# Kernel tuning notes

Measured on AMD Instinct MI355X. Metric: run time of the kernel, lower is better.

The kernel has to match this reference:

```python
import jax, jax.numpy as jnp
import numpy as np

D_MODEL = 1024
N_HEADS = 16
D_K = D_MODEL // N_HEADS

def setup_inputs() -> dict:
    key = jax.random.key(0)
    ks = jax.random.split(key, 9)
    s = 1.0 / np.sqrt(D_MODEL)
    inp = {"x": jax.random.normal(ks[0], (2, 2048, D_MODEL), dtype=jnp.float32)}
    for i, name in enumerate(["q", "k", "v", "o"]):
        inp[f"W{name}"] = jax.random.uniform(ks[1 + i], (D_MODEL, D_MODEL), dtype=jnp.float32, minval=-s, maxval=s)
        inp[f"b{name}"] = jax.random.uniform(ks[5 + i], (D_MODEL,), dtype=jnp.float32, minval=-s, maxval=s)
    return inp

def _split_heads(t):
    B, S, _ = t.shape
    return t.reshape(B, S, N_HEADS, D_K).transpose(0, 2, 1, 3)  # [B,H,S,d_k]

def reference(x, Wq, bq, Wk, bk, Wv, bv, Wo, bo):
    # QKV projections (torch Linear: x @ W.T + b)
    q = _split_heads(x @ Wq.T + bq)
    k = _split_heads(x @ Wk.T + bk)
    v = _split_heads(x @ Wv.T + bv)
    scores = jnp.einsum('bhqd,bhkd->bhqk', q, k) / jnp.sqrt(jnp.asarray(D_K, x.dtype))
    probs = jax.nn.softmax(scores, axis=-1)
    attn = jnp.einsum('bhqk,bhkd->bhqd', probs, v)  # [B,H,S,d_k]
    B, H, S, _ = attn.shape
    merged = attn.transpose(0, 2, 1, 3).reshape(B, S, D_MODEL)
    return merged @ Wo.T + bo
```

## Files before the change

kernel.cpp:

```cpp
#include <hip/hip_runtime.h>
#include <hip/hip_bf16.h>
#include <stdint.h>


#define LOG2E 1.4426950408889634f

typedef float f32x4 __attribute__((ext_vector_type(4)));
typedef float f32x16 __attribute__((ext_vector_type(16)));
typedef short bf16x8 __attribute__((ext_vector_type(8)));
typedef short bf16x4 __attribute__((ext_vector_type(4)));
typedef unsigned int u32x2 __attribute__((ext_vector_type(2)));

__device__ __forceinline__ unsigned short f2bf(float f) {
  __hip_bfloat16 h = __float2bfloat16(f);
  return reinterpret_cast<unsigned short&>(h);
}

#define GLDS(g, l) __builtin_amdgcn_global_load_lds(                          \
    (const __attribute__((address_space(1))) void*)(g),                       \
    (__attribute__((address_space(3))) void*)(l), 16, 0, 0)

__global__ __launch_bounds__(256) void k_conv(const float* __restrict__ src,
                                              unsigned short* __restrict__ dst,
                                              int n4, float scale) {
  int i = blockIdx.x * 256 + threadIdx.x;
  const int stride = gridDim.x * 256;
  for (; i < n4; i += stride) {
    float4 v = ((const float4*)src)[i];
    ushort4 o;
    o.x = f2bf(v.x * scale);
    o.y = f2bf(v.y * scale);
    o.z = f2bf(v.z * scale);
    o.w = f2bf(v.w * scale);
    ((ushort4*)dst)[i] = o;
  }
}

__global__ __launch_bounds__(256) void k_convW(const float* __restrict__ wq,
                                               const float* __restrict__ wk,
                                               const float* __restrict__ wv,
                                               const float* __restrict__ wo,
                                               unsigned short* __restrict__ dq,
                                               unsigned short* __restrict__ dk,
                                               unsigned short* __restrict__ dv,
                                               unsigned short* __restrict__ dw) {
  const int m = blockIdx.y;
  const float* src = (m == 0) ? wq : (m == 1) ? wk : (m == 2) ? wv : wo;
  unsigned short* dst = (m == 0) ? dq : (m == 1) ? dk : (m == 2) ? dv : dw;
  const float scale = (m == 0) ? (0.125f * LOG2E) : 1.0f;
  int i = blockIdx.x * 256 + threadIdx.x;
  float4 v = ((const float4*)src)[i];
  ushort4 o;
  o.x = f2bf(v.x * scale);
  o.y = f2bf(v.y * scale);
  o.z = f2bf(v.z * scale);
  o.w = f2bf(v.w * scale);
  ((ushort4*)dst)[i] = o;
}

__global__ __launch_bounds__(256) void k_bias(const float* __restrict__ bq,
                                              const float* __restrict__ bk,
                                              const float* __restrict__ bv,
                                              float* __restrict__ out) {
  int i = blockIdx.x * 256 + threadIdx.x;
  float v;
  if (i < 1024) v = bq[i] * (0.125f * LOG2E);
  else if (i < 2048) v = bk[i - 1024];
  else v = bv[i - 2048];
  out[i] = v;
}

template <int MODE>
__global__ __launch_bounds__(256) void k_gemm(const unsigned short* __restrict__ A,
                                              const unsigned short* __restrict__ B,
                                              const float* __restrict__ bias,
                                              void* __restrict__ outp) {
  __shared__ unsigned short As[128 * 32];
  __shared__ unsigned short Bs[128 * 32];
  const int tid = threadIdx.x;
  const int lane = tid & 63, wid = tid >> 6;
  const int wr = wid >> 1, wc = wid & 1;
  const int r = lane & 15, g = lane >> 4;
  const int bm = blockIdx.x, bn = blockIdx.y;

  const unsigned short* gA = A + (size_t)bm * 128 * 1024;
  const unsigned short* gB = B + (size_t)bn * 128 * 1024;
  const int row0 = tid >> 2, cg = (tid & 3) * 8;

  f32x4 acc[4][4] = {};

  for (int k0 = 0; k0 < 1024; k0 += 32) {
    __syncthreads();
    GLDS(gA + (size_t)row0 * 1024 + k0 + cg,        As + row0 * 32 + cg);
    GLDS(gA + (size_t)(row0 + 64) * 1024 + k0 + cg, As + (row0 + 64) * 32 + cg);
    GLDS(gB + (size_t)row0 * 1024 + k0 + cg,        Bs + row0 * 32 + cg);
    GLDS(gB + (size_t)(row0 + 64) * 1024 + k0 + cg, Bs + (row0 + 64) * 32 + cg);
    __syncthreads();

    bf16x8 af[4], bfr[4];
#pragma unroll
    for (int i = 0; i < 4; i++) {
      af[i]  = *(const bf16x8*)(As + (wr * 64 + i * 16 + r) * 32 + g * 8);
      bfr[i] = *(const bf16x8*)(Bs + (wc * 64 + i * 16 + r) * 32 + g * 8);
    }
#pragma unroll
    for (int i = 0; i < 4; i++)
#pragma unroll
      for (int j = 0; j < 4; j++)
        acc[i][j] = __builtin_amdgcn_mfma_f32_16x16x32_bf16(af[i], bfr[j], acc[i][j], 0, 0, 0);
  }

#pragma unroll
  for (int i = 0; i < 4; i++) {
    const int rowb = bm * 128 + wr * 64 + i * 16 + g * 4;
#pragma unroll
    for (int j = 0; j < 4; j++) {
      const int col = bn * 128 + wc * 64 + j * 16 + r;
      const float bv = bias[col];
#pragma unroll
      for (int t = 0; t < 4; t++) {
        const int row = rowb + t;
        const float val = acc[i][j][t] + bv;
        if (MODE == 0) {
          const int mat = col >> 10, nn = col & 1023;
          const int hh = nn >> 6, dd = nn & 63;
          const int bb = row >> 11, ss = row & 2047;
          size_t idx;
          if (mat == 2)
            idx = (size_t)2 * 4194304 + (size_t)((bb * 16 + hh) * 64 + dd) * 2048 + ss;
          else
            idx = (size_t)mat * 4194304 + (size_t)((bb * 16 + hh) * 2048 + ss) * 64 + dd;
          ((unsigned short*)outp)[idx] = f2bf(val);
        } else {
          ((float*)outp)[(size_t)row * 1024 + col] = val;
        }
      }
    }
  }
}

__global__ __launch_bounds__(256) void k_attn(const unsigned short* __restrict__ Q,
                                              const unsigned short* __restrict__ Km,
                                              const unsigned short* __restrict__ Vt,
                                              unsigned short* __restrict__ merged) {
  __shared__ unsigned short Kb[2][4096];
  __shared__ unsigned short Vb[2][4096];
  const int tid = threadIdx.x;
  const int lane = tid & 63, w = tid >> 6;
  const int l31 = lane & 31, hi = lane >> 5;
  const int bh = blockIdx.y;
  const int b = bh >> 4, h = bh & 15;
  const int q0 = blockIdx.x * 128;

  const unsigned short* Qh  = Q  + (size_t)bh * 131072;
  const unsigned short* Kh  = Km + (size_t)bh * 131072;
  const unsigned short* Vth = Vt + (size_t)bh * 131072;

  const int qrow = q0 + w * 32 + l31;
  bf16x8 bQ[4];
#pragma unroll
  for (int c = 0; c < 4; c++)
    bQ[c] = *(const bf16x8*)(Qh + (size_t)qrow * 64 + c * 16 + hi * 8);

  int ksrc[2], vsrc[2];
#pragma unroll
  for (int op = 0; op < 2; op++) {
    const int ck = op * 256 + tid;
    const int s = ck >> 8, c = (ck >> 6) & 3, l2 = ck & 63;
    ksrc[op] = (s * 32 + (l2 & 31)) * 64 + c * 16 + (l2 >> 5) * 8;
    vsrc[op] = (s * 32 + (l2 & 31)) * 2048 + c * 16 + (l2 >> 5) * 8;
  }
  const int ldst = tid * 8;

  GLDS(Kh + ksrc[0],  &Kb[0][ldst]);
  GLDS(Kh + ksrc[1],  &Kb[0][2048 + ldst]);
  GLDS(Vth + vsrc[0], &Vb[0][ldst]);
  GLDS(Vth + vsrc[1], &Vb[0][2048 + ldst]);
  __syncthreads();

  f32x16 o0 = {0.f,0.f,0.f,0.f,0.f,0.f,0.f,0.f,0.f,0.f,0.f,0.f,0.f,0.f,0.f,0.f};
  f32x16 o1 = o0;
  float lsum = 0.f;

  for (int t = 0; t < 32; ++t) {
    const int cur = t & 1;
    if (t < 31) {
      const size_t kv = (size_t)(t + 1) * 64;
      GLDS(Kh + kv * 64 + ksrc[0],  &Kb[cur ^ 1][ldst]);
      GLDS(Kh + kv * 64 + ksrc[1],  &Kb[cur ^ 1][2048 + ldst]);
      GLDS(Vth + kv + vsrc[0], &Vb[cur ^ 1][ldst]);
      GLDS(Vth + kv + vsrc[1], &Vb[cur ^ 1][2048 + ldst]);
    }

    bf16x8 kf[2][4], vf[2][4];
#pragma unroll
    for (int s = 0; s < 2; s++)
#pragma unroll
      for (int c = 0; c < 4; c++) {
        kf[s][c] = *(const bf16x8*)(&Kb[cur][((s * 4 + c) * 64 + lane) * 8]);
        vf[s][c] = *(const bf16x8*)(&Vb[cur][((s * 4 + c) * 64 + lane) * 8]);
      }

    f32x16 z = {0.f,0.f,0.f,0.f,0.f,0.f,0.f,0.f,0.f,0.f,0.f,0.f,0.f,0.f,0.f,0.f};
    f32x16 St0 = z, St1 = z;
#pragma unroll
    for (int c = 0; c < 4; c++) {
      St0 = __builtin_amdgcn_mfma_f32_32x32x16_bf16(kf[0][c], bQ[c], St0, 0, 0, 0);
      St1 = __builtin_amdgcn_mfma_f32_32x32x16_bf16(kf[1][c], bQ[c], St1, 0, 0, 0);
    }

    float p0[16], p1[16];
    float ps = 0.f;
#pragma unroll
    for (int u = 0; u < 16; u++) {
      p0[u] = __builtin_amdgcn_exp2f(St0[u]);
      p1[u] = __builtin_amdgcn_exp2f(St1[u]);
      ps += p0[u] + p1[u];
    }
    lsum += ps;

#pragma unroll
    for (int c = 0; c < 4; c++) {
      const float* pp = (c < 2) ? p0 : p1;
      const int R = (c & 1) * 8;
      unsigned int a0, a1, b0, b1;
      asm("v_cvt_pk_bf16_f32 %0, %1, %2" : "=v"(a0) : "v"(pp[R + 0]), "v"(pp[R + 1]));
      asm("v_cvt_pk_bf16_f32 %0, %1, %2" : "=v"(a1) : "v"(pp[R + 2]), "v"(pp[R + 3]));
      asm("v_cvt_pk_bf16_f32 %0, %1, %2" : "=v"(b0) : "v"(pp[R + 4]), "v"(pp[R + 5]));
      asm("v_cvt_pk_bf16_f32 %0, %1, %2" : "=v"(b1) : "v"(pp[R + 6]), "v"(pp[R + 7]));
      u32x2 r0 = __builtin_amdgcn_permlane32_swap(a0, b0, false, false);
      u32x2 r1 = __builtin_amdgcn_permlane32_swap(a1, b1, false, false);
      union { unsigned int u[4]; bf16x8 v; } pf;
      pf.u[0] = r0[0]; pf.u[1] = r1[0]; pf.u[2] = r0[1]; pf.u[3] = r1[1];
      o0 = __builtin_amdgcn_mfma_f32_32x32x16_bf16(vf[0][c], pf.v, o0, 0, 0, 0);
      o1 = __builtin_amdgcn_mfma_f32_32x32x16_bf16(vf[1][c], pf.v, o1, 0, 0, 0);
    }

    __syncthreads();
  }

  const float inv = 1.0f / (lsum + __shfl_xor(lsum, 32));
  const size_t base = (size_t)(b * 2048 + qrow) * 1024 + h * 64;
#pragma unroll
  for (int ds = 0; ds < 2; ds++) {
    const f32x16& oo = ds ? o1 : o0;
#pragma unroll
    for (int m = 0; m < 4; m++) {
      bf16x4 ov;
#pragma unroll
      for (int i = 0; i < 4; i++) ov[i] = (short)f2bf(oo[m * 4 + i] * inv);
      *(bf16x4*)(&merged[base + ds * 32 + m * 8 + hi * 4]) = ov;
    }
  }
}

extern "C" void kernel_launch(void* const* d_in, const int* in_sizes, int n_in,
                              void* d_out, int out_size, void* d_ws, size_t ws_size,
                              hipStream_t stream) {
  const float* x  = (const float*)d_in[0];
  const float* Wq = (const float*)d_in[1];
  const float* bq = (const float*)d_in[2];
  const float* Wk = (const float*)d_in[3];
  const float* bk = (const float*)d_in[4];
  const float* Wv = (const float*)d_in[5];
  const float* bv = (const float*)d_in[6];
  const float* Wo = (const float*)d_in[7];
  const float* bo = (const float*)d_in[8];

  if (ws_size < (size_t)50343936) return;

  unsigned short* ws  = (unsigned short*)d_ws;
  unsigned short* xb  = ws;
  unsigned short* Wb  = ws + 4194304;
  unsigned short* Wob = ws + 7340032;
  unsigned short* qkv = ws + 8388608;
  unsigned short* mrg = ws + 20971520;
  float* biasQ = (float*)(ws + 25165824);

  k_conv<<<dim3(2048), dim3(256), 0, stream>>>(x, xb, 1048576, 1.0f);
  k_convW<<<dim3(1024, 4), dim3(256), 0, stream>>>(Wq, Wk, Wv, Wo,
      Wb, Wb + 1048576, Wb + 2097152, Wob);
  k_bias<<<dim3(12), dim3(256), 0, stream>>>(bq, bk, bv, biasQ);

  k_gemm<0><<<dim3(32, 24), dim3(256), 0, stream>>>(xb, Wb, biasQ, (void*)qkv);
  k_attn<<<dim3(16, 32), dim3(256), 0, stream>>>(qkv, qkv + 4194304, qkv + 8388608, mrg);
  k_gemm<1><<<dim3(32, 8), dim3(256), 0, stream>>>(mrg, Wob, bo, d_out);
}
```

Before: 134.0 us.

## Split attention KV range across two warp groups with LDS reduction

The attention kernel now launches 512 threads per block, and two groups of four waves each process half of the key/value sequence for the same 128 query rows. Partial outputs and row sums are combined through a swizzled LDS buffer before normalization and store. The inner loop is also restructured into per-32-key subtiles to cut live registers. This doubles waves per block to hide latency, at the cost of more LDS, an extra reduction phase and block-wide barriers shared by both groups.

```diff
diff --git a/kernel.cpp b/kernel.cpp
--- a/kernel.cpp
+++ b/kernel.cpp
@@ -139,22 +139,23 @@
   }
 }
 
-__global__ __launch_bounds__(256) void k_attn(const unsigned short* __restrict__ Q,
-                                              const unsigned short* __restrict__ Km,
-                                              const unsigned short* __restrict__ Vt,
-                                              unsigned short* __restrict__ merged) {
-  __shared__ unsigned short Kb[2][4096];
-  __shared__ unsigned short Vb[2][4096];
+__global__ __launch_bounds__(512, 4) void k_attn(const unsigned short* __restrict__ Q,
+                                                 const unsigned short* __restrict__ Km,
+                                                 const unsigned short* __restrict__ Vt,
+                                                 unsigned short* __restrict__ merged) {
+  __shared__ unsigned short Kb[2][2][4096];
+  __shared__ unsigned short Vb[2][2][4096];
   const int tid = threadIdx.x;
-  const int lane = tid & 63, w = tid >> 6;
+  const int kg = tid >> 8, gtid = tid & 255;
+  const int lane = tid & 63, w = (tid >> 6) & 3;
   const int l31 = lane & 31, hi = lane >> 5;
   const int bh = blockIdx.y;
   const int b = bh >> 4, h = bh & 15;
   const int q0 = blockIdx.x * 128;
 
   const unsigned short* Qh  = Q  + (size_t)bh * 131072;
-  const unsigned short* Kh  = Km + (size_t)bh * 131072;
-  const unsigned short* Vth = Vt + (size_t)bh * 131072;
+  const unsigned short* KhG = Km + (size_t)bh * 131072 + (size_t)kg * 65536;
+  const unsigned short* VtG = Vt + (size_t)bh * 131072 + 1024 * kg;
 
   const int qrow = q0 + w * 32 + l31;
   bf16x8 bQ[4];
@@ -165,91 +166,132 @@
   int ksrc[2], vsrc[2];
 #pragma unroll
   for (int op = 0; op < 2; op++) {
-    const int ck = op * 256 + tid;
+    const int ck = op * 256 + gtid;
     const int s = ck >> 8, c = (ck >> 6) & 3, l2 = ck & 63;
     ksrc[op] = (s * 32 + (l2 & 31)) * 64 + c * 16 + (l2 >> 5) * 8;
     vsrc[op] = (s * 32 + (l2 & 31)) * 2048 + c * 16 + (l2 >> 5) * 8;
   }
-  const int ldst = tid * 8;
-
-  GLDS(Kh + ksrc[0],  &Kb[0][ldst]);
-  GLDS(Kh + ksrc[1],  &Kb[0][2048 + ldst]);
-  GLDS(Vth + vsrc[0], &Vb[0][ldst]);
-  GLDS(Vth + vsrc[1], &Vb[0][2048 + ldst]);
+  const int ldst = gtid * 8;
+
+  GLDS(KhG + ksrc[0], &Kb[kg][0][ldst]);
+  GLDS(KhG + ksrc[1], &Kb[kg][0][2048 + ldst]);
+  GLDS(VtG + vsrc[0], &Vb[kg][0][ldst]);
+  GLDS(VtG + vsrc[1], &Vb[kg][0][2048 + ldst]);
   __syncthreads();
 
   f32x16 o0 = {0.f,0.f,0.f,0.f,0.f,0.f,0.f,0.f,0.f,0.f,0.f,0.f,0.f,0.f,0.f,0.f};
   f32x16 o1 = o0;
   float lsum = 0.f;
 
-  for (int t = 0; t < 32; ++t) {
+  for (int t = 0; t < 16; ++t) {
     const int cur = t & 1;
-    if (t < 31) {
+    if (t < 15) {
       const size_t kv = (size_t)(t + 1) * 64;
-      GLDS(Kh + kv * 64 + ksrc[0],  &Kb[cur ^ 1][ldst]);
-      GLDS(Kh + kv * 64 + ksrc[1],  &Kb[cur ^ 1][2048 + ldst]);
-      GLDS(Vth + kv + vsrc[0], &Vb[cur ^ 1][ldst]);
-      GLDS(Vth + kv + vsrc[1], &Vb[cur ^ 1][2048 + ldst]);
-    }
-
-    bf16x8 kf[2][4], vf[2][4];
-#pragma unroll
-    for (int s = 0; s < 2; s++)
-#pragma unroll
-      for (int c = 0; c < 4; c++) {
-        kf[s][c] = *(const bf16x8*)(&Kb[cur][((s * 4 + c) * 64 + lane) * 8]);
-        vf[s][c] = *(const bf16x8*)(&Vb[cur][((s * 4 + c) * 64 + lane) * 8]);
+      GLDS(KhG + kv * 64 + ksrc[0], &Kb[kg][cur ^ 1][ldst]);
+      GLDS(KhG + kv * 64 + ksrc[1], &Kb[kg][cur ^ 1][2048 + ldst]);
+      GLDS(VtG + kv + vsrc[0], &Vb[kg][cur ^ 1][ldst]);
+      GLDS(VtG + kv + vsrc[1], &Vb[kg][cur ^ 1][2048 + ldst]);
+    }
+
+    const unsigned short* kb = &Kb[kg][cur][0];
+    const unsigned short* vb = &Vb[kg][cur][0];
+
+#define SUBTILE(SC)                                                            \
+    {                                                                          \
+      bf16x8 kf0 = *(const bf16x8*)(kb + (((SC)*4 + 0) * 64 + lane) * 8);      \
+      bf16x8 kf1 = *(const bf16x8*)(kb + (((SC)*4 + 1) * 64 + lane) * 8);      \
+      bf16x8 kf2 = *(const bf16x8*)(kb + (((SC)*4 + 2) * 64 + lane) * 8);      \
+      bf16x8 kf3 = *(const bf16x8*)(kb + (((SC)*4 + 3) * 64 + lane) * 8);      \
+      f32x16 St = {0.f,0.f,0.f,0.f,0.f,0.f,0.f,0.f,                            \
+                   0.f,0.f,0.f,0.f,0.f,0.f,0.f,0.f};                           \
+      St = __builtin_amdgcn_mfma_f32_32x32x16_bf16(kf0, bQ[0], St, 0, 0, 0);   \
+      St = __builtin_amdgcn_mfma_f32_32x32x16_bf16(kf1, bQ[1], St, 0, 0, 0);   \
+      St = __builtin_amdgcn_mfma_f32_32x32x16_bf16(kf2, bQ[2], St, 0, 0, 0);   \
+      St = __builtin_amdgcn_mfma_f32_32x32x16_bf16(kf3, bQ[3], St, 0, 0, 0);   \
+      float p[16];                                                             \
+      float ps = 0.f;                                                          \
+      _Pragma("unroll")                                                        \
+      for (int u = 0; u < 16; u++) {                                           \
+        p[u] = __builtin_amdgcn_exp2f(St[u]);                                  \
+        ps += p[u];                                                            \
+      }                                                                        \
+      lsum += ps;                                                              \
+      unsigned int a0, a1, b0, b1;                                             \
+      asm("v_cvt_pk_bf16_f32 %0, %1, %2" : "=v"(a0) : "v"(p[0]), "v"(p[1]));   \
+      asm("v_cvt_pk_bf16_f32 %0, %1, %2" : "=v"(a1) : "v"(p[2]), "v"(p[3]));   \
+      asm("v_cvt_pk_bf16_f32 %0, %1, %2" : "=v"(b0) : "v"(p[4]), "v"(p[5]));   \
+      asm("v_cvt_pk_bf16_f32 %0, %1, %2" : "=v"(b1) : "v"(p[6]), "v"(p[7]));   \
+      u32x2 r0 = __builtin_amdgcn_permlane32_swap(a0, b0, false, false);       \
+      u32x2 r1 = __builtin_amdgcn_permlane32_swap(a1, b1, false, false);       \
+      union { unsigned int u[4]; bf16x8 v; } pfE;                              \
+      pfE.u[0] = r0[0]; pfE.u[1] = r1[0]; pfE.u[2] = r0[1]; pfE.u[3] = r1[1];  \
+      asm("v_cvt_pk_bf16_f32 %0, %1, %2" : "=v"(a0) : "v"(p[8]), "v"(p[9]));   \
+      asm("v_cvt_pk_bf16_f32 %0, %1, %2" : "=v"(a1) : "v"(p[10]), "v"(p[11])); \
+      asm("v_cvt_pk_bf16_f32 %0, %1, %2" : "=v"(b0) : "v"(p[12]), "v"(p[13])); \
+      asm("v_cvt_pk_bf16_f32 %0, %1, %2" : "=v"(b1) : "v"(p[14]), "v"(p[15])); \
+      r0 = __builtin_amdgcn_permlane32_swap(a0, b0, false, false);             \
+      r1 = __builtin_amdgcn_permlane32_swap(a1, b1, false, false);             \
+      union { unsigned int u[4]; bf16x8 v; } pfO;                              \
+      pfO.u[0] = r0[0]; pfO.u[1] = r1[0]; pfO.u[2] = r0[1]; pfO.u[3] = r1[1];  \
+      bf16x8 v00 = *(const bf16x8*)(vb + ((0 + 2*(SC)) * 64 + lane) * 8);      \
+      bf16x8 v01 = *(const bf16x8*)(vb + ((1 + 2*(SC)) * 64 + lane) * 8);      \
+      bf16x8 v10 = *(const bf16x8*)(vb + ((4 + 2*(SC)) * 64 + lane) * 8);      \
+      bf16x8 v11 = *(const bf16x8*)(vb + ((5 + 2*(SC)) * 64 + lane) * 8);      \
+      o0 = __builtin_amdgcn_mfma_f32_32x32x16_bf16(v00, pfE.v, o0, 0, 0, 0);   \
+      o0 = __builtin_amdgcn_mfma_f32_32x32x16_bf16(v01, pfO.v, o0, 0, 0, 0);   \
+      o1 = __builtin_amdgcn_mfma_f32_32x32x16_bf16(v10, pfE.v, o1, 0, 0, 0);   \
+      o1 = __builtin_amdgcn_mfma_f32_32x32x16_bf16(v11, pfO.v, o1, 0, 0, 0);   \
+    }
+
+    SUBTILE(0)
+    SUBTILE(1)
+#undef SUBTILE
+
+    __syncthreads();
+  }
+
+  float* lbuf = (float*)&Vb[0][0][0];
+  char*  ob   = (char*)&Kb[0][0][0] + gtid * 128;
+  const unsigned sw2 = ((unsigned)(gtid & 7)) << 4;
+  if (kg == 1) {
+#pragma unroll
+    for (int j = 0; j < 4; j++) {
+      float4 t0 = { o0[4*j], o0[4*j+1], o0[4*j+2], o0[4*j+3] };
+      *(float4*)(ob + (((unsigned)(j * 16)) ^ sw2)) = t0;
+    }
+#pragma unroll
+    for (int j = 0; j < 4; j++) {
+      float4 t1 = { o1[4*j], o1[4*j+1], o1[4*j+2], o1[4*j+3] };
+      *(float4*)(ob + (((unsigned)(64 + j * 16)) ^ sw2)) = t1;
+    }
+    lbuf[gtid] = lsum;
+  }
+  __syncthreads();
+  if (kg == 0) {
+#pragma unroll
+    for (int j = 0; j < 4; j++) {
+      float4 t0 = *(const float4*)(ob + (((unsigned)(j * 16)) ^ sw2));
+      o0[4*j] += t0.x; o0[4*j+1] += t0.y; o0[4*j+2] += t0.z; o0[4*j+3] += t0.w;
+    }
+#pragma unroll
+    for (int j = 0; j < 4; j++) {
+      float4 t1 = *(const float4*)(ob + (((unsigned)(64 + j * 16)) ^ sw2));
+      o1[4*j] += t1.x; o1[4*j+1] += t1.y; o1[4*j+2] += t1.z; o1[4*j+3] += t1.w;
+    }
+    lsum += lbuf[gtid];
+
+    const float inv = 1.0f / (lsum + __shfl_xor(lsum, 32));
+    const size_t base = (size_t)(b * 2048 + qrow) * 1024 + h * 64;
+#pragma unroll
+    for (int ds = 0; ds < 2; ds++) {
+      const f32x16& oo = ds ? o1 : o0;
+#pragma unroll
+      for (int m = 0; m < 4; m++) {
+        bf16x4 ov;
+#pragma unroll
+        for (int i = 0; i < 4; i++) ov[i] = (short)f2bf(oo[m * 4 + i] * inv);
+        *(bf16x4*)(&merged[base + ds * 32 + m * 8 + hi * 4]) = ov;
       }
-
-    f32x16 z = {0.f,0.f,0.f,0.f,0.f,0.f,0.f,0.f,0.f,0.f,0.f,0.f,0.f,0.f,0.f,0.f};
-    f32x16 St0 = z, St1 = z;
-#pragma unroll
-    for (int c = 0; c < 4; c++) {
-      St0 = __builtin_amdgcn_mfma_f32_32x32x16_bf16(kf[0][c], bQ[c], St0, 0, 0, 0);
-      St1 = __builtin_amdgcn_mfma_f32_32x32x16_bf16(kf[1][c], bQ[c], St1, 0, 0, 0);
-    }
-
-    float p0[16], p1[16];
-    float ps = 0.f;
-#pragma unroll
-    for (int u = 0; u < 16; u++) {
-      p0[u] = __builtin_amdgcn_exp2f(St0[u]);
-      p1[u] = __builtin_amdgcn_exp2f(St1[u]);
-      ps += p0[u] + p1[u];
-    }
-    lsum += ps;
-
-#pragma unroll
-    for (int c = 0; c < 4; c++) {
-      const float* pp = (c < 2) ? p0 : p1;
-      const int R = (c & 1) * 8;
-      unsigned int a0, a1, b0, b1;
-      asm("v_cvt_pk_bf16_f32 %0, %1, %2" : "=v"(a0) : "v"(pp[R + 0]), "v"(pp[R + 1]));
-      asm("v_cvt_pk_bf16_f32 %0, %1, %2" : "=v"(a1) : "v"(pp[R + 2]), "v"(pp[R + 3]));
-      asm("v_cvt_pk_bf16_f32 %0, %1, %2" : "=v"(b0) : "v"(pp[R + 4]), "v"(pp[R + 5]));
-      asm("v_cvt_pk_bf16_f32 %0, %1, %2" : "=v"(b1) : "v"(pp[R + 6]), "v"(pp[R + 7]));
-      u32x2 r0 = __builtin_amdgcn_permlane32_swap(a0, b0, false, false);
-      u32x2 r1 = __builtin_amdgcn_permlane32_swap(a1, b1, false, false);
-      union { unsigned int u[4]; bf16x8 v; } pf;
-      pf.u[0] = r0[0]; pf.u[1] = r1[0]; pf.u[2] = r0[1]; pf.u[3] = r1[1];
-      o0 = __builtin_amdgcn_mfma_f32_32x32x16_bf16(vf[0][c], pf.v, o0, 0, 0, 0);
-      o1 = __builtin_amdgcn_mfma_f32_32x32x16_bf16(vf[1][c], pf.v, o1, 0, 0, 0);
-    }
-
-    __syncthreads();
-  }
-
-  const float inv = 1.0f / (lsum + __shfl_xor(lsum, 32));
-  const size_t base = (size_t)(b * 2048 + qrow) * 1024 + h * 64;
-#pragma unroll
-  for (int ds = 0; ds < 2; ds++) {
-    const f32x16& oo = ds ? o1 : o0;
-#pragma unroll
-    for (int m = 0; m < 4; m++) {
-      bf16x4 ov;
-#pragma unroll
-      for (int i = 0; i < 4; i++) ov[i] = (short)f2bf(oo[m * 4 + i] * inv);
-      *(bf16x4*)(&merged[base + ds * 32 + m * 8 + hi * 4]) = ov;
     }
   }
 }
@@ -283,6 +325,6 @@
   k_bias<<<dim3(12), dim3(256), 0, stream>>>(bq, bk, bv, biasQ);
 
   k_gemm<0><<<dim3(32, 24), dim3(256), 0, stream>>>(xb, Wb, biasQ, (void*)qkv);
-  k_attn<<<dim3(16, 32), dim3(256), 0, stream>>>(qkv, qkv + 4194304, qkv + 8388608, mrg);
+  k_attn<<<dim3(16, 32), dim3(512), 0, stream>>>(qkv, qkv + 4194304, qkv + 8388608, mrg);
   k_gemm<1><<<dim3(32, 8), dim3(256), 0, stream>>>(mrg, Wob, bo, d_out);
 }
```

New measurement: 136.2 us. About the same (+1.7%).
